# Performance work log

Hardware: AMD Instinct MI355X
Metric: run time of the kernel (lower is better)

## Reference

```python
import jax, jax.numpy as jnp
import numpy as np

TEMPERATURE = 0.5


def setup_inputs() -> dict:
    key = jax.random.key(0)
    k1, k2 = jax.random.split(key)
    N, D = 4096, 256
    z_i = jax.random.normal(k1, (N, D), dtype=jnp.float32)
    z_j = jax.random.normal(k2, (N, D), dtype=jnp.float32)
    return {"z_i": z_i, "z_j": z_j}


def reference(z_i, z_j):
    N = z_i.shape[0]
    z = jnp.concatenate([z_i, z_j], axis=0)            # (2N, D)
    sim = (z @ z.T) / TEMPERATURE                       # (2N, 2N)
    # mask self-similarity on the diagonal
    diag = jnp.eye(2 * N, dtype=bool)
    sim = jnp.where(diag, -jnp.inf, sim)
    # positive pair labels: i <-> i+N
    labels = jnp.concatenate([jnp.arange(N, 2 * N), jnp.arange(0, N)])
    logp = jax.nn.log_softmax(sim, axis=-1)             # (2N, 2N)
    loss = -jnp.mean(jnp.take_along_axis(logp, labels[:, None], axis=-1))
    return loss
```

## Files before the change

kernel.cpp:

```cpp
#include <hip/hip_runtime.h>
#include <hip/hip_bf16.h>


typedef __bf16 bf16x8 __attribute__((ext_vector_type(8)));
typedef __bf16 bf16x4 __attribute__((ext_vector_type(4)));
typedef float  f32x16 __attribute__((ext_vector_type(16)));

#define NPAIR 4096
#define NROW  8192
#define DIM   256
#define STRIPS 8
#define RBLK  16384
#define SQSCALE 1.6986437f
#define LN2F    0.6931471805599453f
#define M2      176.0f

__global__ __launch_bounds__(256) void k_convert(const float* __restrict__ zi,
                                                 const float* __restrict__ zj,
                                                 __bf16* __restrict__ Zf,
                                                 float* __restrict__ pos,
                                                 float* __restrict__ out) {
    const int w = threadIdx.x >> 6, lane = threadIdx.x & 63;
    const int r = blockIdx.x * 4 + w;
    if (blockIdx.x == 0 && threadIdx.x == 0) out[0] = 0.0f;
    const float4 vi = *(const float4*)(zi + r * DIM + lane * 4);
    const float4 vj = *(const float4*)(zj + r * DIM + lane * 4);
    bf16x4 bi, bj;
    bi[0] = (__bf16)(vi.x * SQSCALE); bi[1] = (__bf16)(vi.y * SQSCALE);
    bi[2] = (__bf16)(vi.z * SQSCALE); bi[3] = (__bf16)(vi.w * SQSCALE);
    bj[0] = (__bf16)(vj.x * SQSCALE); bj[1] = (__bf16)(vj.y * SQSCALE);
    bj[2] = (__bf16)(vj.z * SQSCALE); bj[3] = (__bf16)(vj.w * SQSCALE);
    const int t = lane >> 2, h = (lane >> 1) & 1, inner = (lane & 1) * 8;
    char* Zb = (char*)Zf;
    *(bf16x4*)(Zb + (size_t)(r >> 5) * RBLK + t * 1024 + h * 512 + (r & 31) * 16 + inner) = bi;
    const int r2 = r + NPAIR;
    *(bf16x4*)(Zb + (size_t)(r2 >> 5) * RBLK + t * 1024 + h * 512 + (r2 & 31) * 16 + inner) = bj;
    float d = vi.x * vj.x + vi.y * vj.y + vi.z * vj.z + vi.w * vj.w;
    #pragma unroll
    for (int m = 32; m >= 1; m >>= 1) d += __shfl_xor(d, m);
    if (lane == 0) pos[r] = 2.0f * d;
}

__global__ __launch_bounds__(512) void k_lse(const __bf16* __restrict__ Zf,
                                             float* __restrict__ Lpart) {
    const int strip = blockIdx.x >> 6;
    const int rb    = blockIdx.x & 63;
    const int tid   = threadIdx.x;
    const int wave  = tid >> 6;
    const int wr    = wave & 3;
    const int wc    = wave >> 2;
    const int lane  = tid & 63, lm = lane & 31, half = lane >> 5;
    const int laneoff = half * 512 + lm * 16;

    __shared__ char smem[65536];
    {
        const char* src = (const char*)Zf + (size_t)rb * 4 * RBLK + tid * 16;
        char* dst = smem + tid * 16;
        #pragma unroll
        for (int it = 0; it < 8; it++)
            *(int4*)(dst + it * 8192) = *(const int4*)(src + it * 8192);
    }
    __syncthreads();

    const char* Bl    = smem + wr * RBLK + laneoff;
    const char* Abase = (const char*)Zf + (size_t)(strip * 32 + wc * 2) * RBLK + laneoff;
    const int rowblk  = rb * 4 + wr;

    float l = 0.0f;

    for (int ph = 0; ph < 8; ph++) {
        const char* Ap = Abase + (size_t)ph * 4 * RBLK;
        f32x16 acc0 = (f32x16)(0.0f);
        f32x16 acc1 = (f32x16)(0.0f);

        bf16x8 a0 = *(const bf16x8*)(Ap);
        bf16x8 a1 = *(const bf16x8*)(Ap + RBLK);
        bf16x8 b  = *(const bf16x8*)(Bl);
        #pragma unroll
        for (int t = 0; t < 16; t++) {
            bf16x8 na0, na1, nb;
            if (t < 15) {
                na0 = *(const bf16x8*)(Ap + (t + 1) * 1024);
                na1 = *(const bf16x8*)(Ap + RBLK + (t + 1) * 1024);
                nb  = *(const bf16x8*)(Bl + (t + 1) * 1024);
            }
            acc0 = __builtin_amdgcn_mfma_f32_32x32x16_bf16(a0, b, acc0, 0, 0, 0);
            acc1 = __builtin_amdgcn_mfma_f32_32x32x16_bf16(a1, b, acc1, 0, 0, 0);
            a0 = na0; a1 = na1; b = nb;
        }

        const int cb0 = strip * 32 + ph * 4 + wc * 2;
        float ssum = 0.0f;
        if (cb0 == rowblk) {
            #pragma unroll
            for (int rg = 0; rg < 16; rg++) {
                const int c_local = (rg & 3) + 8 * (rg >> 2) + 4 * half;
                ssum += (c_local == lm) ? 0.0f : __builtin_exp2f(acc0[rg] - M2);
            }
        } else {
            #pragma unroll
            for (int rg = 0; rg < 16; rg++) ssum += __builtin_exp2f(acc0[rg] - M2);
        }
        if (cb0 + 1 == rowblk) {
            #pragma unroll
            for (int rg = 0; rg < 16; rg++) {
                const int c_local = (rg & 3) + 8 * (rg >> 2) + 4 * half;
                ssum += (c_local == lm) ? 0.0f : __builtin_exp2f(acc1[rg] - M2);
            }
        } else {
            #pragma unroll
            for (int rg = 0; rg < 16; rg++) ssum += __builtin_exp2f(acc1[rg] - M2);
        }
        l += ssum;
    }

    l += __shfl_xor(l, 32);

    __syncthreads();
    float* part = (float*)smem;
    if (half == 0) part[wc * 128 + wr * 32 + lm] = l;
    __syncthreads();
    if (tid < 128)
        Lpart[strip * NROW + rb * 128 + tid] = part[tid] + part[128 + tid];
}

__global__ __launch_bounds__(256) void k_final(const float* __restrict__ Lpart,
                                               const float* __restrict__ pos,
                                               float* __restrict__ out) {
    __shared__ float red[256];
    const int t = threadIdx.x;
    const int r = blockIdx.x * 256 + t;
    float l = 0.0f;
    #pragma unroll
    for (int s = 0; s < STRIPS; s++) l += Lpart[s * NROW + r];
    const float lse = (M2 + __builtin_log2f(l)) * LN2F;
    red[t] = lse - pos[r & (NPAIR - 1)];
    __syncthreads();
    for (int ofs = 128; ofs > 0; ofs >>= 1) {
        if (t < ofs) red[t] += red[t + ofs];
        __syncthreads();
    }
    if (t == 0) atomicAdd(out, red[0] / (float)NROW);
}

extern "C" void kernel_launch(void* const* d_in, const int* in_sizes, int n_in,
                              void* d_out, int out_size, void* d_ws, size_t ws_size,
                              hipStream_t stream) {
    const float* zi = (const float*)d_in[0];
    const float* zj = (const float*)d_in[1];
    __bf16* Zf   = (__bf16*)d_ws;
    float* pos   = (float*)((char*)d_ws + (size_t)NROW * DIM * 2);
    float* Lpart = pos + NPAIR;

    k_convert<<<NPAIR / 4, 256, 0, stream>>>(zi, zj, Zf, pos, (float*)d_out);
    k_lse<<<64 * STRIPS, 512, 0, stream>>>(Zf, Lpart);
    k_final<<<NROW / 256, 256, 0, stream>>>(Lpart, pos, (float*)d_out);
}
```

Baseline: 106.4 us.

## Use 2x2 MFMA register tile per wave and interleave strip block order

```diff
diff --git a/kernel.cpp b/kernel.cpp
--- a/kernel.cpp
+++ b/kernel.cpp
@@ -43,12 +43,12 @@
 
 __global__ __launch_bounds__(512) void k_lse(const __bf16* __restrict__ Zf,
                                              float* __restrict__ Lpart) {
-    const int strip = blockIdx.x >> 6;
-    const int rb    = blockIdx.x & 63;
+    const int strip = blockIdx.x & 7;
+    const int rb    = blockIdx.x >> 3;
     const int tid   = threadIdx.x;
     const int wave  = tid >> 6;
-    const int wr    = wave & 3;
-    const int wc    = wave >> 2;
+    const int wr    = wave & 1;
+    const int wc    = wave >> 1;
     const int lane  = tid & 63, lm = lane & 31, half = lane >> 5;
     const int laneoff = half * 512 + lm * 16;
 
@@ -62,66 +62,68 @@
     }
     __syncthreads();
 
-    const char* Bl    = smem + wr * RBLK + laneoff;
-    const char* Abase = (const char*)Zf + (size_t)(strip * 32 + wc * 2) * RBLK + laneoff;
-    const int rowblk  = rb * 4 + wr;
+    const char* Bl = smem + (size_t)(wr * 2) * RBLK + laneoff;
+    const char* Ab = (const char*)Zf
+                   + (size_t)(strip * 32 + wc * 2) * RBLK + laneoff;
+    const int rowblk0 = rb * 4 + wr * 2;
 
-    float l = 0.0f;
+    float l0 = 0.0f, l1 = 0.0f;
 
-    for (int ph = 0; ph < 8; ph++) {
-        const char* Ap = Abase + (size_t)ph * 4 * RBLK;
-        f32x16 acc0 = (f32x16)(0.0f);
-        f32x16 acc1 = (f32x16)(0.0f);
+    for (int ph = 0; ph < 4; ph++) {
+        const char* Ap = Ab + (size_t)ph * 8 * RBLK;
+        f32x16 acc00 = (f32x16)(0.0f);
+        f32x16 acc01 = (f32x16)(0.0f);
+        f32x16 acc10 = (f32x16)(0.0f);
+        f32x16 acc11 = (f32x16)(0.0f);
 
         bf16x8 a0 = *(const bf16x8*)(Ap);
         bf16x8 a1 = *(const bf16x8*)(Ap + RBLK);
-        bf16x8 b  = *(const bf16x8*)(Bl);
+        bf16x8 b0 = *(const bf16x8*)(Bl);
+        bf16x8 b1 = *(const bf16x8*)(Bl + RBLK);
         #pragma unroll
         for (int t = 0; t < 16; t++) {
-            bf16x8 na0, na1, nb;
+            bf16x8 na0, na1, nb0, nb1;
             if (t < 15) {
                 na0 = *(const bf16x8*)(Ap + (t + 1) * 1024);
                 na1 = *(const bf16x8*)(Ap + RBLK + (t + 1) * 1024);
-                nb  = *(const bf16x8*)(Bl + (t + 1) * 1024);
+                nb0 = *(const bf16x8*)(Bl + (t + 1) * 1024);
+                nb1 = *(const bf16x8*)(Bl + RBLK + (t + 1) * 1024);
             }
-            acc0 = __builtin_amdgcn_mfma_f32_32x32x16_bf16(a0, b, acc0, 0, 0, 0);
-            acc1 = __builtin_amdgcn_mfma_f32_32x32x16_bf16(a1, b, acc1, 0, 0, 0);
-            a0 = na0; a1 = na1; b = nb;
+            acc00 = __builtin_amdgcn_mfma_f32_32x32x16_bf16(a0, b0, acc00, 0, 0, 0);
+            acc01 = __builtin_amdgcn_mfma_f32_32x32x16_bf16(a0, b1, acc01, 0, 0, 0);
+            acc10 = __builtin_amdgcn_mfma_f32_32x32x16_bf16(a1, b0, acc10, 0, 0, 0);
+            acc11 = __builtin_amdgcn_mfma_f32_32x32x16_bf16(a1, b1, acc11, 0, 0, 0);
+            a0 = na0; a1 = na1; b0 = nb0; b1 = nb1;
         }
 
-        const int cb0 = strip * 32 + ph * 4 + wc * 2;
-        float ssum = 0.0f;
-        if (cb0 == rowblk) {
-            #pragma unroll
-            for (int rg = 0; rg < 16; rg++) {
-                const int c_local = (rg & 3) + 8 * (rg >> 2) + 4 * half;
-                ssum += (c_local == lm) ? 0.0f : __builtin_exp2f(acc0[rg] - M2);
-            }
-        } else {
-            #pragma unroll
-            for (int rg = 0; rg < 16; rg++) ssum += __builtin_exp2f(acc0[rg] - M2);
+        const int cb0 = strip * 32 + ph * 8 + wc * 2;
+        float s00 = 0.0f, s01 = 0.0f, s10 = 0.0f, s11 = 0.0f;
+        #pragma unroll
+        for (int rg = 0; rg < 16; rg++) {
+            const int c_local = (rg & 3) + 8 * (rg >> 2) + 4 * half;
+            const bool dmask = (c_local == lm);
+            s00 += (dmask && cb0     == rowblk0    ) ? 0.0f : __builtin_exp2f(acc00[rg] - M2);
+            s01 += (dmask && cb0     == rowblk0 + 1) ? 0.0f : __builtin_exp2f(acc01[rg] - M2);
+            s10 += (dmask && cb0 + 1 == rowblk0    ) ? 0.0f : __builtin_exp2f(acc10[rg] - M2);
+            s11 += (dmask && cb0 + 1 == rowblk0 + 1) ? 0.0f : __builtin_exp2f(acc11[rg] - M2);
         }
-        if (cb0 + 1 == rowblk) {
-            #pragma unroll
-            for (int rg = 0; rg < 16; rg++) {
-                const int c_local = (rg & 3) + 8 * (rg >> 2) + 4 * half;
-                ssum += (c_local == lm) ? 0.0f : __builtin_exp2f(acc1[rg] - M2);
-            }
-        } else {
-            #pragma unroll
-            for (int rg = 0; rg < 16; rg++) ssum += __builtin_exp2f(acc1[rg] - M2);
-        }
-        l += ssum;
+        l0 += s00 + s10;
+        l1 += s01 + s11;
     }
 
-    l += __shfl_xor(l, 32);
+    l0 += __shfl_xor(l0, 32);
+    l1 += __shfl_xor(l1, 32);
 
     __syncthreads();
     float* part = (float*)smem;
-    if (half == 0) part[wc * 128 + wr * 32 + lm] = l;
+    if (half == 0) {
+        part[wc * 128 + (wr * 2 + 0) * 32 + lm] = l0;
+        part[wc * 128 + (wr * 2 + 1) * 32 + lm] = l1;
+    }
     __syncthreads();
     if (tid < 128)
-        Lpart[strip * NROW + rb * 128 + tid] = part[tid] + part[128 + tid];
+        Lpart[strip * NROW + rb * 128 + tid] =
+            part[tid] + part[128 + tid] + part[256 + tid] + part[384 + tid];
 }
 
 __global__ __launch_bounds__(256) void k_final(const float* __restrict__ Lpart,
```

Result: slower. 116.3 us (+9.3%).
